# Optimization experiments

Hardware: AMD Instinct MI355X
Metric: run time of the kernel (lower is better)

## Reference

```python
import jax, jax.numpy as jnp
import numpy as np

T, B, I, H = 2048, 32, 512, 512


def setup_inputs() -> dict:
    key = jax.random.key(0)
    ks = jax.random.split(key, 8)
    s = 1.0 / np.sqrt(H)
    return {
        "X": jax.random.normal(ks[0], (T, B, I), dtype=jnp.float32),
        "h": jax.random.normal(ks[1], (B, H), dtype=jnp.float32),
        "W_ih": jax.random.uniform(ks[2], (3 * H, I), jnp.float32, -s, s),
        "W_hh": jax.random.uniform(ks[3], (3 * H, H), jnp.float32, -s, s),
        "b_ih": jax.random.uniform(ks[4], (3 * H,), jnp.float32, -s, s),
        "b_hh": jax.random.uniform(ks[5], (3 * H,), jnp.float32, -s, s),
        "W_dense": jax.random.uniform(ks[6], (H, I), jnp.float32, -s, s),
        "b_dense": jax.random.uniform(ks[7], (H,), jnp.float32, -s, s),
    }


def reference(X, h, W_ih, W_hh, b_ih, b_hh, W_dense, b_dense):
    # Precompute input-side gate projections for all timesteps: [T, B, 3H]
    gi_all = jnp.einsum('tbi,gi->tbg', X, W_ih) + b_ih

    def step(h, gi):
        # hidden-side gates for this step: [B, 3H]
        gh = h @ W_hh.T + b_hh
        i_r, i_z, i_n = jnp.split(gi, 3, axis=-1)
        h_r, h_z, h_n = jnp.split(gh, 3, axis=-1)
        r = jax.nn.sigmoid(i_r + h_r)
        z = jax.nn.sigmoid(i_z + h_z)
        n = jnp.tanh(i_n + r * h_n)
        h_new = (1.0 - z) * n + z * h
        return h_new, h_new

    h_last, outputs = jax.lax.scan(step, h, gi_all)
    # AddNorm with dropout=0 (eval): dense(X) + outputs
    dense = jnp.einsum('tbi,hi->tbh', X, W_dense) + b_dense
    return outputs + dense, h_last
```

## Files before the change

### kernel.cpp

```cpp
#include <hip/hip_runtime.h>

#define TT   2048
#define NB   32
#define NI   512
#define NHID 512
#define NWG  32
#define KSL  16

typedef float    f32x4 __attribute__((ext_vector_type(4)));
typedef _Float16 f16x8 __attribute__((ext_vector_type(8)));

__device__ __align__(256) unsigned int g_flags[576];
__device__ __align__(256) _Float16    g_hb0[NB * NHID];
__device__ __align__(256) _Float16    g_hb1[NB * NHID];
__device__ __align__(256) _Float16    g_wfrag[NWG][4][16][64][8];

__device__ __forceinline__ f16x8 pack8(f32x4 a, f32x4 b) {
    f16x8 r;
    r[0] = (_Float16)a[0]; r[1] = (_Float16)a[1]; r[2] = (_Float16)a[2]; r[3] = (_Float16)a[3];
    r[4] = (_Float16)b[0]; r[5] = (_Float16)b[1]; r[6] = (_Float16)b[2]; r[7] = (_Float16)b[3];
    return r;
}

__device__ __forceinline__ unsigned int poll_load_nt(const unsigned int* p) {
    unsigned int v;
    asm volatile("global_load_dword %0, %1, off nt\n\ts_waitcnt vmcnt(0)"
                 : "=v"(v) : "v"(p) : "memory");
    return v;
}

extern "C" __global__ void init_flags_k() {
    for (int i = threadIdx.x; i < 576; i += 256) g_flags[i] = 0u;
}

extern "C" __global__ void pack_wfrag_k(const float* __restrict__ Wih,
                                        const float* __restrict__ Wd) {
    const int w    = blockIdx.x;
    const int tid  = threadIdx.x;
    const int lane = tid & 63;
    const int mat  = tid >> 6;
    const int r15  = lane & 15;
    const int g4   = lane >> 4;
    const float* src = (mat < 3) ? (Wih + (size_t)(mat * 512 + w * KSL + r15) * NI)
                                 : (Wd  + (size_t)(w * KSL + r15) * NI);
    #pragma unroll
    for (int kc = 0; kc < 16; ++kc) {
        const f32x4* p = (const f32x4*)(src + kc * 32 + g4 * 8);
        *(f16x8*)&g_wfrag[w][mat][kc][lane][0] = pack8(p[0], p[1]);
    }
}

extern "C" __global__ void __launch_bounds__(256, 1)
gru_persist(const float* __restrict__ X, const float* __restrict__ h0,
            const float* __restrict__ Wih, const float* __restrict__ Whh,
            const float* __restrict__ bih, const float* __restrict__ bhh,
            const float* __restrict__ Wd,  const float* __restrict__ bd,
            float* __restrict__ out)
{
    if (blockIdx.x & 7) return;
    const int w  = blockIdx.x >> 3;
    const int ks = w * KSL;

    __shared__ _Float16 fragWhh[3][16][64][8];
    __shared__ float    gi_lds[4][2][4][16][20];
    __shared__ float    bias_h[3][KSL];
    __shared__ float    bias_i[4][KSL];
    __shared__ unsigned int seq[16];
    __shared__ unsigned int fast_sh;
    volatile unsigned int* vseq = seq;

    const int tid  = threadIdx.x;
    const int lane = tid & 63;
    const int wv   = tid >> 6;
    const int half = wv & 1;
    const int isp  = wv >> 1;
    const int r15  = lane & 15;
    const int g4   = lane >> 4;

    if (tid < 16) seq[tid] = 0u;
    if (tid < KSL) {
        int k = ks + tid;
        bias_h[0][tid] = bhh[k];
        bias_h[1][tid] = bhh[512 + k];
        bias_h[2][tid] = bhh[1024 + k];
        bias_i[0][tid] = bih[k];
        bias_i[1][tid] = bih[512 + k];
        bias_i[2][tid] = bih[1024 + k];
        bias_i[3][tid] = bd[k];
    }
    if (wv < 3) {
        const float* src = Whh + (size_t)(wv * 512 + ks + r15) * NHID;
        #pragma unroll
        for (int kc = 0; kc < 16; ++kc) {
            const f32x4* p = (const f32x4*)(src + kc * 32 + g4 * 8);
            *(f16x8*)&fragWhh[wv][kc][lane][0] = pack8(p[0], p[1]);
        }
    }
    if (tid == 0) {
        unsigned int xcc;
        asm volatile("s_getreg_b32 %0, hwreg(HW_REG_XCC_ID, 0, 32)" : "=s"(xcc));
        unsigned int bit = 1u << (xcc & 7);
        unsigned int* mask  = g_flags + 512;
        unsigned int* count = g_flags + 513;
        unsigned int old = __hip_atomic_fetch_or(mask, bit, __ATOMIC_RELAXED,
                                                 __HIP_MEMORY_SCOPE_AGENT);
        asm volatile("" :: "v"(old));
        __hip_atomic_fetch_add(count, 1u, __ATOMIC_RELAXED, __HIP_MEMORY_SCOPE_AGENT);
        while (__hip_atomic_load(count, __ATOMIC_RELAXED,
                                 __HIP_MEMORY_SCOPE_AGENT) < NWG) { }
        unsigned int m = __hip_atomic_load(mask, __ATOMIC_RELAXED,
                                           __HIP_MEMORY_SCOPE_AGENT);
        fast_sh = ((m & (m - 1)) == 0) ? 1u : 0u;
    }
    __syncthreads();
    const bool fast = (fast_sh != 0);
    const int  bg   = half * 16 + r15;

    if (!isp) {
        __builtin_amdgcn_s_setprio(1);
        f32x4 hold = *(const f32x4*)(h0 + (size_t)bg * NHID + ks + g4 * 4);
        const f32x4 bhr = *(const f32x4*)&bias_h[0][g4 * 4];
        const f32x4 bhz = *(const f32x4*)&bias_h[1][g4 * 4];
        const f32x4 bhn = *(const f32x4*)&bias_h[2][g4 * 4];
        const f32x4 bir = *(const f32x4*)&bias_i[0][g4 * 4];
        const f32x4 biz = *(const f32x4*)&bias_i[1][g4 * 4];
        const f32x4 bin = *(const f32x4*)&bias_i[2][g4 * 4];
        const f32x4 bd4 = *(const f32x4*)&bias_i[3][g4 * 4];
        const float* h0row = h0 + (size_t)bg * NHID;

        float s0 = 1.0f + 0.5f * (float)tid, s1 = s0 + .3f, s2 = s0 + .6f, s3 = s0 + .9f;
        const float mm = 1.0000001f, cc = 1.0e-7f;

        #pragma unroll 1
        for (int t = 0; t < TT; ++t) {
            if (t > 0 && lane < NWG) {
                const unsigned int* fp = &g_flags[lane * 16 + half * 8];
                if (fast) { while (poll_load_nt(fp) < (unsigned)t) { } }
                else      { while (__hip_atomic_load(fp, __ATOMIC_RELAXED,
                                       __HIP_MEMORY_SCOPE_AGENT) < (unsigned)t) { } }
            }
            f16x8 Bf[16];
            if (t == 0) {
                #pragma unroll
                for (int kc = 0; kc < 16; ++kc) {
                    const f32x4* p = (const f32x4*)(h0row + kc * 32 + g4 * 8);
                    Bf[kc] = pack8(p[0], p[1]);
                }
            } else {
                const _Float16* hrow = ((t & 1) ? g_hb1 : g_hb0) + (size_t)bg * NHID;
                if (fast) {
                    #pragma unroll
                    for (int kc = 0; kc < 16; ++kc) {
                        const _Float16* p = hrow + kc * 32 + g4 * 8;
                        asm volatile("global_load_dwordx4 %0, %1, off nt"
                                     : "=v"(Bf[kc]) : "v"(p));
                    }
                } else {
                    #pragma unroll
                    for (int kc = 0; kc < 16; ++kc) {
                        const _Float16* p = hrow + kc * 32 + g4 * 8;
                        asm volatile("global_load_dwordx4 %0, %1, off sc0 sc1"
                                     : "=v"(Bf[kc]) : "v"(p));
                    }
                }
                asm volatile("s_waitcnt vmcnt(0)" ::: "memory");
                __builtin_amdgcn_sched_barrier(0);
            }
            f32x4 a0 = {0.f,0.f,0.f,0.f}, a1 = a0, a2 = a0;
            #pragma unroll
            for (int kc = 0; kc < 16; ++kc) {
                f16x8 w0 = *(const f16x8*)&fragWhh[0][kc][lane][0];
                f16x8 w1 = *(const f16x8*)&fragWhh[1][kc][lane][0];
                f16x8 w2 = *(const f16x8*)&fragWhh[2][kc][lane][0];
                a0 = __builtin_amdgcn_mfma_f32_16x16x32_f16(w0, Bf[kc], a0, 0, 0, 0);
                a1 = __builtin_amdgcn_mfma_f32_16x16x32_f16(w1, Bf[kc], a1, 0, 0, 0);
                a2 = __builtin_amdgcn_mfma_f32_16x16x32_f16(w2, Bf[kc], a2, 0, 0, 0);
            }
            while (vseq[half] < (unsigned)(t + 1)) {
                #pragma unroll
                for (int i = 0; i < 8; ++i) {
                    s0 = __builtin_fmaf(s0, mm, cc); s1 = __builtin_fmaf(s1, mm, cc);
                    s2 = __builtin_fmaf(s2, mm, cc); s3 = __builtin_fmaf(s3, mm, cc);
                }
            }
            const int par = t & 3;
            f32x4 gr = *(const f32x4*)&gi_lds[par][half][0][r15][g4 * 4];
            f32x4 gz = *(const f32x4*)&gi_lds[par][half][1][r15][g4 * 4];
            f32x4 gn = *(const f32x4*)&gi_lds[par][half][2][r15][g4 * 4];
            f32x4 gd = *(const f32x4*)&gi_lds[par][half][3][r15][g4 * 4];
            asm volatile("s_waitcnt lgkmcnt(0)" ::: "memory");
            if (lane == 0) vseq[2 + half] = (unsigned)(t + 1);
            f32x4 hn, o;
            #pragma unroll
            for (int i = 0; i < 4; ++i) {
                float rr = 1.f / (1.f + __expf(-((gr[i] + bir[i]) + (a0[i] + bhr[i]))));
                float zz = 1.f / (1.f + __expf(-((gz[i] + biz[i]) + (a1[i] + bhz[i]))));
                float aa = (gn[i] + bin[i]) + rr * (a2[i] + bhn[i]);
                float nn = 1.f - 2.f / (__expf(2.f * aa) + 1.f);
                hn[i] = (1.f - zz) * nn + zz * hold[i];
                o[i]  = hn[i] + gd[i] + bd4[i];
            }
            hold = hn;
            union { _Float16 h[4]; unsigned long long u; } cv;
            cv.h[0] = (_Float16)hn[0]; cv.h[1] = (_Float16)hn[1];
            cv.h[2] = (_Float16)hn[2]; cv.h[3] = (_Float16)hn[3];
            _Float16* hw = (((t + 1) & 1) ? g_hb1 : g_hb0) + (size_t)bg * NHID + ks + g4 * 4;
            if (fast) {
                *(unsigned long long*)hw = cv.u;
            } else {
                asm volatile("global_store_dwordx2 %0, %1, off sc0 sc1"
                             :: "v"(hw), "v"(cv.u) : "memory");
            }
            asm volatile("s_waitcnt vmcnt(0)" ::: "memory");
            if (lane == 0) {
                unsigned int* fp = &g_flags[w * 16 + half * 8];
                if (fast) *(volatile unsigned int*)fp = (unsigned)(t + 1);
                else __hip_atomic_store(fp, (unsigned)(t + 1), __ATOMIC_RELAXED,
                                        __HIP_MEMORY_SCOPE_AGENT);
            }
            *(f32x4*)(out + (size_t)t * (NB * NHID) + (size_t)bg * NHID + ks + g4 * 4) = o;
        }
        *(f32x4*)(out + (size_t)TT * (NB * NHID) + (size_t)bg * NHID + ks + g4 * 4) = hold;
        asm volatile("" :: "v"(s0), "v"(s1), "v"(s2), "v"(s3));
    } else {
        __builtin_amdgcn_s_setprio(1);
        const float* Xrow = X + (size_t)bg * NI;

        f16x8 zf = {};
        f32x4 accd = {0.f, 0.f, 0.f, 0.f};

        #pragma unroll 1
        for (int tp = 0; tp < TT; ++tp) {
            while ((int)vseq[2 + half] < tp - 3) {
                accd = __builtin_amdgcn_mfma_f32_16x16x32_f16(zf, zf, accd, 0, 0, 0);
                accd = __builtin_amdgcn_mfma_f32_16x16x32_f16(zf, zf, accd, 0, 0, 0);
                accd = __builtin_amdgcn_mfma_f32_16x16x32_f16(zf, zf, accd, 0, 0, 0);
                accd = __builtin_amdgcn_mfma_f32_16x16x32_f16(zf, zf, accd, 0, 0, 0);
            }
            const float* xp = Xrow + (size_t)tp * (NB * NI);
            f16x8 Bf[16];
            #pragma unroll
            for (int kc = 0; kc < 16; ++kc) {
                const f32x4* p = (const f32x4*)(xp + kc * 32 + g4 * 8);
                Bf[kc] = pack8(p[0], p[1]);
            }
            f32x4 acc[4];
            #pragma unroll
            for (int q = 0; q < 4; ++q) acc[q] = (f32x4){0.f, 0.f, 0.f, 0.f};
            #pragma unroll
            for (int mat = 0; mat < 4; ++mat) {
                f16x8 wb[16];
                #pragma unroll
                for (int kc = 0; kc < 16; ++kc)
                    wb[kc] = *(const f16x8*)&g_wfrag[w][mat][kc][lane][0];
                #pragma unroll
                for (int kc = 0; kc < 16; ++kc)
                    acc[mat] = __builtin_amdgcn_mfma_f32_16x16x32_f16(wb[kc], Bf[kc], acc[mat], 0, 0, 0);
            }
            const int par = tp & 3;
            *(f32x4*)&gi_lds[par][half][0][r15][g4 * 4] = acc[0];
            *(f32x4*)&gi_lds[par][half][1][r15][g4 * 4] = acc[1];
            *(f32x4*)&gi_lds[par][half][2][r15][g4 * 4] = acc[2];
            *(f32x4*)&gi_lds[par][half][3][r15][g4 * 4] = acc[3];
            asm volatile("s_waitcnt lgkmcnt(0)" ::: "memory");
            if (lane == 0) vseq[half] = (unsigned)(tp + 1);
        }
        asm volatile("" :: "v"(accd[0]), "v"(accd[1]), "v"(accd[2]), "v"(accd[3]));
    }
}

extern "C" void kernel_launch(void* const* d_in, const int* in_sizes, int n_in,
                              void* d_out, int out_size, void* d_ws, size_t ws_size,
                              hipStream_t stream) {
    const float* X   = (const float*)d_in[0];
    const float* h0  = (const float*)d_in[1];
    const float* Wih = (const float*)d_in[2];
    const float* Whh = (const float*)d_in[3];
    const float* bih = (const float*)d_in[4];
    const float* bhh = (const float*)d_in[5];
    const float* Wd  = (const float*)d_in[6];
    const float* bd  = (const float*)d_in[7];
    float* out = (float*)d_out;

    init_flags_k<<<dim3(1), dim3(256), 0, stream>>>();
    pack_wfrag_k<<<dim3(NWG), dim3(256), 0, stream>>>(Wih, Wd);

    gru_persist<<<dim3(256), dim3(256), 0, stream>>>(
        X, h0, Wih, Whh, bih, bhh, Wd, bd, out);
}
```

Baseline: 10.28 ms.

## Stage W_ih fragments in LDS and move MFMA clock-warming spin into recurrent waves

Three of the four input-projection weight matrices are now packed into shared memory at kernel start, so the projection waves read them from LDS rather than reloading them from global memory every timestep. Only the dense weights are still read from global. The projection MFMAs are interleaved across the four output matrices. The dummy-MFMA busy loop, likely meant to keep the clock up, moves from the projection waves' wait into the recurrent waves' flag poll, which now uses a wave-wide __all check. This adds 48KB of LDS and extra MFMA issue pressure while the recurrent waves spin.

```diff
diff --git a/kernel.cpp b/kernel.cpp
--- a/kernel.cpp
+++ b/kernel.cpp
@@ -62,6 +62,7 @@
     const int ks = w * KSL;
 
     __shared__ _Float16 fragWhh[3][16][64][8];
+    __shared__ _Float16 fragWih[3][16][64][8];
     __shared__ float    gi_lds[4][2][4][16][20];
     __shared__ float    bias_h[3][KSL];
     __shared__ float    bias_i[4][KSL];
@@ -88,12 +89,15 @@
         bias_i[2][tid] = bih[1024 + k];
         bias_i[3][tid] = bd[k];
     }
-    if (wv < 3) {
-        const float* src = Whh + (size_t)(wv * 512 + ks + r15) * NHID;
+    for (int s = wv; s < 6; s += 4) {
+        const float* src = (s < 3) ? (Whh + (size_t)(s * 512 + ks + r15) * NHID)
+                                   : (Wih + (size_t)((s - 3) * 512 + ks + r15) * NI);
         #pragma unroll
         for (int kc = 0; kc < 16; ++kc) {
             const f32x4* p = (const f32x4*)(src + kc * 32 + g4 * 8);
-            *(f16x8*)&fragWhh[wv][kc][lane][0] = pack8(p[0], p[1]);
+            f16x8 v = pack8(p[0], p[1]);
+            if (s < 3) *(f16x8*)&fragWhh[s][kc][lane][0] = v;
+            else       *(f16x8*)&fragWih[s - 3][kc][lane][0] = v;
         }
     }
     if (tid == 0) {
@@ -130,14 +134,31 @@
 
         float s0 = 1.0f + 0.5f * (float)tid, s1 = s0 + .3f, s2 = s0 + .6f, s3 = s0 + .9f;
         const float mm = 1.0000001f, cc = 1.0e-7f;
+        f16x8 zf = {};
+        f32x4 d0 = {0.f,0.f,0.f,0.f}, d1 = d0, d2 = d0, d3 = d0;
 
         #pragma unroll 1
         for (int t = 0; t < TT; ++t) {
-            if (t > 0 && lane < NWG) {
+            if (t > 0) {
                 const unsigned int* fp = &g_flags[lane * 16 + half * 8];
-                if (fast) { while (poll_load_nt(fp) < (unsigned)t) { } }
-                else      { while (__hip_atomic_load(fp, __ATOMIC_RELAXED,
-                                       __HIP_MEMORY_SCOPE_AGENT) < (unsigned)t) { } }
+                for (;;) {
+                    int rdy = 1;
+                    if (lane < NWG) {
+                        unsigned v = fast ? poll_load_nt(fp)
+                                          : __hip_atomic_load(fp, __ATOMIC_RELAXED,
+                                                              __HIP_MEMORY_SCOPE_AGENT);
+                        rdy = (v >= (unsigned)t);
+                    }
+                    if (__all(rdy)) break;
+                    #pragma unroll
+                    for (int i = 0; i < 8; ++i) {
+                        d0 = __builtin_amdgcn_mfma_f32_16x16x32_f16(zf, zf, d0, 0, 0, 0);
+                        d1 = __builtin_amdgcn_mfma_f32_16x16x32_f16(zf, zf, d1, 0, 0, 0);
+                        d2 = __builtin_amdgcn_mfma_f32_16x16x32_f16(zf, zf, d2, 0, 0, 0);
+                        d3 = __builtin_amdgcn_mfma_f32_16x16x32_f16(zf, zf, d3, 0, 0, 0);
+                    }
+                }
+                asm volatile("" ::: "memory");
             }
             f16x8 Bf[16];
             if (t == 0) {
@@ -222,21 +243,18 @@
         }
         *(f32x4*)(out + (size_t)TT * (NB * NHID) + (size_t)bg * NHID + ks + g4 * 4) = hold;
         asm volatile("" :: "v"(s0), "v"(s1), "v"(s2), "v"(s3));
+        asm volatile("" :: "v"(d0[0]), "v"(d1[0]), "v"(d2[0]), "v"(d3[0]));
     } else {
         __builtin_amdgcn_s_setprio(1);
         const float* Xrow = X + (size_t)bg * NI;
 
-        f16x8 zf = {};
-        f32x4 accd = {0.f, 0.f, 0.f, 0.f};
-
         #pragma unroll 1
         for (int tp = 0; tp < TT; ++tp) {
-            while ((int)vseq[2 + half] < tp - 3) {
-                accd = __builtin_amdgcn_mfma_f32_16x16x32_f16(zf, zf, accd, 0, 0, 0);
-                accd = __builtin_amdgcn_mfma_f32_16x16x32_f16(zf, zf, accd, 0, 0, 0);
-                accd = __builtin_amdgcn_mfma_f32_16x16x32_f16(zf, zf, accd, 0, 0, 0);
-                accd = __builtin_amdgcn_mfma_f32_16x16x32_f16(zf, zf, accd, 0, 0, 0);
-            }
+            while ((int)vseq[2 + half] < tp - 3) { }
+            f16x8 wb3[16];
+            #pragma unroll
+            for (int kc = 0; kc < 16; ++kc)
+                wb3[kc] = *(const f16x8*)&g_wfrag[w][3][kc][lane][0];
             const float* xp = Xrow + (size_t)tp * (NB * NI);
             f16x8 Bf[16];
             #pragma unroll
@@ -244,28 +262,25 @@
                 const f32x4* p = (const f32x4*)(xp + kc * 32 + g4 * 8);
                 Bf[kc] = pack8(p[0], p[1]);
             }
-            f32x4 acc[4];
-            #pragma unroll
-            for (int q = 0; q < 4; ++q) acc[q] = (f32x4){0.f, 0.f, 0.f, 0.f};
-            #pragma unroll
-            for (int mat = 0; mat < 4; ++mat) {
-                f16x8 wb[16];
-                #pragma unroll
-                for (int kc = 0; kc < 16; ++kc)
-                    wb[kc] = *(const f16x8*)&g_wfrag[w][mat][kc][lane][0];
-                #pragma unroll
-                for (int kc = 0; kc < 16; ++kc)
-                    acc[mat] = __builtin_amdgcn_mfma_f32_16x16x32_f16(wb[kc], Bf[kc], acc[mat], 0, 0, 0);
+            f32x4 a0 = {0.f,0.f,0.f,0.f}, a1 = a0, a2 = a0, a3 = a0;
+            #pragma unroll
+            for (int kc = 0; kc < 16; ++kc) {
+                f16x8 w0 = *(const f16x8*)&fragWih[0][kc][lane][0];
+                f16x8 w1 = *(const f16x8*)&fragWih[1][kc][lane][0];
+                f16x8 w2 = *(const f16x8*)&fragWih[2][kc][lane][0];
+                a0 = __builtin_amdgcn_mfma_f32_16x16x32_f16(w0, Bf[kc], a0, 0, 0, 0);
+                a1 = __builtin_amdgcn_mfma_f32_16x16x32_f16(w1, Bf[kc], a1, 0, 0, 0);
+                a2 = __builtin_amdgcn_mfma_f32_16x16x32_f16(w2, Bf[kc], a2, 0, 0, 0);
+                a3 = __builtin_amdgcn_mfma_f32_16x16x32_f16(wb3[kc], Bf[kc], a3, 0, 0, 0);
             }
             const int par = tp & 3;
-            *(f32x4*)&gi_lds[par][half][0][r15][g4 * 4] = acc[0];
-            *(f32x4*)&gi_lds[par][half][1][r15][g4 * 4] = acc[1];
-            *(f32x4*)&gi_lds[par][half][2][r15][g4 * 4] = acc[2];
-            *(f32x4*)&gi_lds[par][half][3][r15][g4 * 4] = acc[3];
+            *(f32x4*)&gi_lds[par][half][0][r15][g4 * 4] = a0;
+            *(f32x4*)&gi_lds[par][half][1][r15][g4 * 4] = a1;
+            *(f32x4*)&gi_lds[par][half][2][r15][g4 * 4] = a2;
+            *(f32x4*)&gi_lds[par][half][3][r15][g4 * 4] = a3;
             asm volatile("s_waitcnt lgkmcnt(0)" ::: "memory");
             if (lane == 0) vseq[half] = (unsigned)(tp + 1);
         }
-        asm volatile("" :: "v"(accd[0]), "v"(accd[1]), "v"(accd[2]), "v"(accd[3]));
     }
 }
 
```

After: 16.78 ms. 1.63x slower.
